# Performance work log

Hardware: AMD Instinct MI355X
Metric: run time of the kernel (lower is better)

The kernel has to match this reference:

```python
import jax, jax.numpy as jnp
import numpy as np

D_MODEL = 512
BATCH_A = 8192
MAX_MATCHES = 16
N_B = 100000
D_HID = 2 * D_MODEL  # 1024
D_IN = 2 * D_MODEL   # concat([a, mean_b])


def setup_inputs() -> dict:
    key = jax.random.key(0)
    ks = jax.random.split(key, 10)
    table_a_emb = jax.random.normal(ks[0], (BATCH_A, D_MODEL), dtype=jnp.float32)
    table_b_emb = jax.random.normal(ks[1], (N_B, D_MODEL), dtype=jnp.float32)
    # padded neighbor lists; negative values mark padding / no-match
    match_indices = jax.random.randint(ks[2], (BATCH_A, MAX_MATCHES), -5, N_B, dtype=jnp.int64)
    s_in = 1.0 / np.sqrt(D_IN)
    s_h = 1.0 / np.sqrt(D_HID)
    W_in = jax.random.uniform(ks[3], (D_IN, D_HID), jnp.float32, -s_in, s_in)
    b_in = jax.random.uniform(ks[4], (D_HID,), jnp.float32, -s_in, s_in)
    W_h = jax.random.uniform(ks[5], (D_HID, D_HID), jnp.float32, -s_h, s_h)
    b_h = jax.random.uniform(ks[6], (D_HID,), jnp.float32, -s_h, s_h)
    W_out = jax.random.uniform(ks[7], (D_HID, D_MODEL), jnp.float32, -s_h, s_h)
    b_out = jax.random.uniform(ks[8], (D_MODEL,), jnp.float32, -s_h, s_h)
    return {"table_a_emb": table_a_emb, "table_b_emb": table_b_emb,
            "match_indices": match_indices, "W_in": W_in, "b_in": b_in,
            "W_h": W_h, "b_h": b_h, "W_out": W_out, "b_out": b_out}


def reference(table_a_emb, table_b_emb, match_indices, W_in, b_in, W_h, b_h, W_out, b_out):
    mask = match_indices >= 0                                   # [B, M]
    safe_idx = jnp.where(mask, match_indices, 0)
    gathered = table_b_emb[safe_idx] * mask[..., None].astype(table_b_emb.dtype)  # [B, M, D]
    counts = mask.sum(axis=-1)                                  # [B]
    denom = jnp.maximum(counts, 1).astype(table_b_emb.dtype)[:, None]
    agg_b = gathered.sum(axis=1) / denom                        # [B, D] masked mean
    combined = jnp.concatenate([table_a_emb, agg_b], axis=-1)   # [B, 2D]
    h = jax.nn.relu(combined @ W_in + b_in)
    h = jax.nn.relu(h @ W_h + b_h)
    out = h @ W_out + b_out                                     # [B, D]
    # rows with zero valid matches emit zeros, not MLP(concat(a, 0))
    return jnp.where((counts > 0)[:, None], out, jnp.zeros_like(out))
```

## Files before the change

kernel.cpp:

```cpp
#include <hip/hip_runtime.h>

#define DM 512
#define DI 1024
#define MM 16

typedef __attribute__((ext_vector_type(4))) float f32x4;
typedef __attribute__((ext_vector_type(8))) short short8;
typedef __attribute__((ext_vector_type(8))) unsigned short ushort8;

__device__ __forceinline__ unsigned short f2bf(float x) {
  union { float f; unsigned u; } c; c.f = x;
  unsigned r = (c.u + 0x7fffu + ((c.u >> 16) & 1u)) >> 16;
  return (unsigned short)r;
}

__device__ __forceinline__ void gload_lds16(const void* g, void* l) {
  __builtin_amdgcn_global_load_lds(
      (const __attribute__((address_space(1))) unsigned int*)g,
      (__attribute__((address_space(3))) unsigned int*)l, 16, 0, 0);
}


__device__ __forceinline__ void wt_tile(const float* __restrict__ W,
                                        unsigned short* __restrict__ Wt,
                                        int K, int N, int bx, int by,
                                        float (*tile)[33], int tx, int ty) {
  #pragma unroll
  for (int i = ty; i < 32; i += 8)
    tile[i][tx] = W[(size_t)(by + i) * N + bx + tx];
  __syncthreads();
  #pragma unroll
  for (int i = ty; i < 32; i += 8)
    Wt[(size_t)(bx + i) * K + by + tx] = f2bf(tile[tx][i]);
}

__global__ __launch_bounds__(256)
void prep_kernel(const float* __restrict__ Aemb,
                 const float* __restrict__ Bemb,
                 const int* __restrict__ midx,
                 const float* __restrict__ W_in,
                 const float* __restrict__ W_h,
                 const float* __restrict__ W_out,
                 unsigned short* __restrict__ X,
                 int* __restrict__ counts,
                 unsigned short* __restrict__ Wt_in,
                 unsigned short* __restrict__ Wt_h,
                 unsigned short* __restrict__ Wt_out) {
  __shared__ float tile[32][33];
  const int b = blockIdx.x;
  const int tx = threadIdx.x & 31, ty = threadIdx.x >> 5;
  if (b < 1024) {
    wt_tile(W_in, Wt_in, 1024, 1024, (b & 31) * 32, (b >> 5) * 32, tile, tx, ty);
    return;
  } else if (b < 2048) {
    int lb = b - 1024;
    wt_tile(W_h, Wt_h, 1024, 1024, (lb & 31) * 32, (lb >> 5) * 32, tile, tx, ty);
    return;
  } else if (b < 2560) {
    int lb = b - 2048;
    wt_tile(W_out, Wt_out, 1024, 512, (lb & 15) * 32, (lb >> 4) * 32, tile, tx, ty);
    return;
  }
  int row = __builtin_amdgcn_readfirstlane((b - 2560) * 4 + (threadIdx.x >> 6));
  int l = threadIdx.x & 63;
  float acc[8] = {0,0,0,0,0,0,0,0};
  int cnt = 0;
  const int* ip = midx + row * MM;
  #pragma unroll
  for (int m = 0; m < MM; ++m) {
    int id = ip[m];
    if (id >= 0) {
      ++cnt;
      const f32x4* p = (const f32x4*)(Bemb + (size_t)id * DM) + l * 2;
      f32x4 u = p[0], v = p[1];
      acc[0]+=u[0]; acc[1]+=u[1]; acc[2]+=u[2]; acc[3]+=u[3];
      acc[4]+=v[0]; acc[5]+=v[1]; acc[6]+=v[2]; acc[7]+=v[3];
    }
  }
  float inv = 1.0f / (float)(cnt > 0 ? cnt : 1);
  const f32x4* pa = (const f32x4*)(Aemb + (size_t)row * DM) + l * 2;
  f32x4 a0 = pa[0], a1 = pa[1];
  ushort8 va, vb;
  va[0]=f2bf(a0[0]); va[1]=f2bf(a0[1]); va[2]=f2bf(a0[2]); va[3]=f2bf(a0[3]);
  va[4]=f2bf(a1[0]); va[5]=f2bf(a1[1]); va[6]=f2bf(a1[2]); va[7]=f2bf(a1[3]);
  #pragma unroll
  for (int i = 0; i < 8; ++i) vb[i] = f2bf(acc[i] * inv);
  *(ushort8*)(X + (size_t)row * DI + l * 8) = va;
  *(ushort8*)(X + (size_t)row * DI + DM + l * 8) = vb;
  if (l == 0) counts[row] = cnt;
}

template<int RELU, int FINAL>
__global__ __launch_bounds__(256, 2)
void gemm_kernel(const unsigned short* __restrict__ A,
                 const unsigned short* __restrict__ Bt,
                 const float* __restrict__ bias,
                 unsigned short* __restrict__ Cb,
                 float* __restrict__ Cf,
                 const int* __restrict__ counts,
                 int M, int N, int K) {
  __shared__ __align__(16) unsigned short As[128 * 64];
  __shared__ __align__(16) unsigned short Bs[128 * 64];
  const int t = threadIdx.x;
  const int l = t & 63, w = t >> 6;
  const int wr = w >> 1, wc = w & 1;

  const int nwg = gridDim.x * gridDim.y;
  const int wg = blockIdx.y * gridDim.x + blockIdx.x;
  const int swzid = (wg & 7) * (nwg >> 3) + (wg >> 3);
  const int bx = swzid % gridDim.x, by = swzid / gridDim.x;

  const int blockM = by * 128, blockN = bx * 128;
  const unsigned short* Ab = A + (size_t)blockM * K;
  const unsigned short* Bb = Bt + (size_t)blockN * K;

  f32x4 acc[4][4];
  #pragma unroll
  for (int m = 0; m < 4; ++m)
    #pragma unroll
    for (int n = 0; n < 4; ++n) acc[m][n] = (f32x4){0.f, 0.f, 0.f, 0.f};

  int so_row[4], so_col[4];
  #pragma unroll
  for (int c = 0; c < 4; ++c) {
    int o = c * 4096 + t * 16;
    int row = o >> 7;
    int cb = (o & 127) ^ ((row & 7) << 4);
    so_row[c] = row; so_col[c] = cb >> 1;
  }

  const int r = l & 15, ko = (l >> 4) * 8;
  const int swz = (r & 7) << 4;
  const char* Ac = (const char*)As;
  const char* Bc = (const char*)Bs;
  const int NT = K >> 6;

  #pragma unroll
  for (int c = 0; c < 4; ++c) {
    gload_lds16(Ab + (size_t)so_row[c] * K + so_col[c], (char*)As + c * 4096 + w * 1024);
    gload_lds16(Bb + (size_t)so_row[c] * K + so_col[c], (char*)Bs + c * 4096 + w * 1024);
  }

  for (int kt = 0; kt < NT; ++kt) {
    __syncthreads();
    #pragma unroll
    for (int kk = 0; kk < 64; kk += 32) {
      short8 aF[4], bF[4];
      #pragma unroll
      for (int m = 0; m < 4; ++m) {
        int byteo = ((wr * 64 + m * 16 + r) * 128 + (kk + ko) * 2) ^ swz;
        aF[m] = *(const short8*)(Ac + byteo);
      }
      #pragma unroll
      for (int n = 0; n < 4; ++n) {
        int byteo = ((wc * 64 + n * 16 + r) * 128 + (kk + ko) * 2) ^ swz;
        bF[n] = *(const short8*)(Bc + byteo);
      }
      #pragma unroll
      for (int m = 0; m < 4; ++m)
        #pragma unroll
        for (int n = 0; n < 4; ++n)
          acc[m][n] = __builtin_amdgcn_mfma_f32_16x16x32_bf16(aF[m], bF[n], acc[m][n], 0, 0, 0);
    }
    __syncthreads();
    if (kt + 1 < NT) {
      int k0 = (kt + 1) << 6;
      #pragma unroll
      for (int c = 0; c < 4; ++c) {
        gload_lds16(Ab + (size_t)so_row[c] * K + k0 + so_col[c], (char*)As + c * 4096 + w * 1024);
        gload_lds16(Bb + (size_t)so_row[c] * K + k0 + so_col[c], (char*)Bs + c * 4096 + w * 1024);
      }
    }
  }

  float bn[4];
  #pragma unroll
  for (int n = 0; n < 4; ++n) bn[n] = bias[blockN + wc * 64 + n * 16 + r];
  const int rowBase = blockM + wr * 64 + (l >> 4) * 4;
  #pragma unroll
  for (int m = 0; m < 4; ++m) {
    #pragma unroll
    for (int j = 0; j < 4; ++j) {
      int grow = rowBase + m * 16 + j;
      if (FINAL) {
        float cm = (counts[grow] > 0) ? 1.0f : 0.0f;
        #pragma unroll
        for (int n = 0; n < 4; ++n) {
          float v = (acc[m][n][j] + bn[n]) * cm;
          Cf[(size_t)grow * N + blockN + wc * 64 + n * 16 + r] = v;
        }
      } else {
        #pragma unroll
        for (int n = 0; n < 4; ++n) {
          float v = acc[m][n][j] + bn[n];
          if (RELU) v = v > 0.f ? v : 0.f;
          Cb[(size_t)grow * N + blockN + wc * 64 + n * 16 + r] = f2bf(v);
        }
      }
    }
  }
}

extern "C" void kernel_launch(void* const* d_in, const int* in_sizes, int n_in,
                              void* d_out, int out_size, void* d_ws, size_t ws_size,
                              hipStream_t stream) {
  const float* a_emb = (const float*)d_in[0];
  const float* b_emb = (const float*)d_in[1];
  const int*   midx  = (const int*)d_in[2];
  const float* W_in  = (const float*)d_in[3];
  const float* b_in  = (const float*)d_in[4];
  const float* W_h   = (const float*)d_in[5];
  const float* b_h   = (const float*)d_in[6];
  const float* W_out = (const float*)d_in[7];
  const float* b_out = (const float*)d_in[8];

  char* ws = (char*)d_ws;
  unsigned short* X      = (unsigned short*)(ws);
  unsigned short* H1     = (unsigned short*)(ws + 16777216);
  unsigned short* Wt_in  = (unsigned short*)(ws + 33554432);
  unsigned short* Wt_h   = (unsigned short*)(ws + 35651584);
  unsigned short* Wt_out = (unsigned short*)(ws + 37748736);
  int*            counts = (int*)(ws + 38797312);

  prep_kernel<<<4608, 256, 0, stream>>>(a_emb, b_emb, midx, W_in, W_h, W_out,
                                        X, counts, Wt_in, Wt_h, Wt_out);

  gemm_kernel<1, 0><<<dim3(8, 64), 256, 0, stream>>>(X,  Wt_in,  b_in,  H1, nullptr, nullptr, 8192, 1024, 1024);
  gemm_kernel<1, 0><<<dim3(8, 64), 256, 0, stream>>>(H1, Wt_h,   b_h,   X,  nullptr, nullptr, 8192, 1024, 1024);
  gemm_kernel<0, 1><<<dim3(4, 64), 256, 0, stream>>>(X,  Wt_out, b_out, nullptr, (float*)d_out, counts, 8192, 512, 1024);
}
```

Measured before the change: 114.5 us.

## Overlap gather with A-half of first GEMM via split-K fused kernel

Splits the first layer's K dimension: a fused kernel runs the gather/mean blocks interleaved with GEMM tiles computing table_a @ W_in[:512] (converting fp32 A to bf16 on the fly), storing a bf16 partial. A second GEMM then handles the mean_b half and adds the partial before bias and ReLU. Weight transposition moves to its own kernel. The aim is to overlap memory-bound gather work with matrix work, at the cost of an extra kernel launch, a bf16 round-trip for the partial sum (a precision loss), and extra workspace.

```diff
diff --git a/kernel.cpp b/kernel.cpp
--- a/kernel.cpp
+++ b/kernel.cpp
@@ -13,6 +13,9 @@
   unsigned r = (c.u + 0x7fffu + ((c.u >> 16) & 1u)) >> 16;
   return (unsigned short)r;
 }
+__device__ __forceinline__ float bf2f(unsigned short h) {
+  union { unsigned u; float f; } c; c.u = ((unsigned)h) << 16; return c.f;
+}
 
 __device__ __forceinline__ void gload_lds16(const void* g, void* l) {
   __builtin_amdgcn_global_load_lds(
@@ -20,7 +23,6 @@
       (__attribute__((address_space(3))) unsigned int*)l, 16, 0, 0);
 }
 
-
 __device__ __forceinline__ void wt_tile(const float* __restrict__ W,
                                         unsigned short* __restrict__ Wt,
                                         int K, int N, int bx, int by,
@@ -35,33 +37,150 @@
 }
 
 __global__ __launch_bounds__(256)
-void prep_kernel(const float* __restrict__ Aemb,
-                 const float* __restrict__ Bemb,
-                 const int* __restrict__ midx,
-                 const float* __restrict__ W_in,
-                 const float* __restrict__ W_h,
-                 const float* __restrict__ W_out,
-                 unsigned short* __restrict__ X,
-                 int* __restrict__ counts,
-                 unsigned short* __restrict__ Wt_in,
-                 unsigned short* __restrict__ Wt_h,
-                 unsigned short* __restrict__ Wt_out) {
+void wt_kernel(const float* __restrict__ W_in, const float* __restrict__ W_h,
+               const float* __restrict__ W_out,
+               unsigned short* __restrict__ Wt_in, unsigned short* __restrict__ Wt_h,
+               unsigned short* __restrict__ Wt_out) {
   __shared__ float tile[32][33];
   const int b = blockIdx.x;
   const int tx = threadIdx.x & 31, ty = threadIdx.x >> 5;
-  if (b < 1024) {
-    wt_tile(W_in, Wt_in, 1024, 1024, (b & 31) * 32, (b >> 5) * 32, tile, tx, ty);
+  if (b < 1024)      wt_tile(W_in,  Wt_in,  1024, 1024, (b & 31) * 32, (b >> 5) * 32, tile, tx, ty);
+  else if (b < 2048) { int lb = b - 1024; wt_tile(W_h,  Wt_h,  1024, 1024, (lb & 31) * 32, (lb >> 5) * 32, tile, tx, ty); }
+  else               { int lb = b - 2048; wt_tile(W_out, Wt_out, 1024, 512, (lb & 15) * 32, (lb >> 4) * 32, tile, tx, ty); }
+}
+
+__global__ __launch_bounds__(256, 2)
+void fused_kernel(const float* __restrict__ Aemb,
+                  const float* __restrict__ Bemb,
+                  const int* __restrict__ midx,
+                  const unsigned short* __restrict__ Wt_in,
+                  unsigned short* __restrict__ Xb,
+                  unsigned short* __restrict__ H1accb,
+                  int* __restrict__ counts) {
+  __shared__ __align__(16) unsigned short As[128 * 64];
+  __shared__ __align__(16) unsigned short Bs[128 * 64];
+  const int b = blockIdx.x;
+  const int t = threadIdx.x;
+
+  if (b % 5 != 0) {
+    int gid = b - b / 5 - 1;
+    int row = gid * 4 + (t >> 6);
+    int l = t & 63;
+    float acc[8] = {0,0,0,0,0,0,0,0};
+    int cnt = 0;
+    const int* ip = midx + row * MM;
+    #pragma unroll
+    for (int m = 0; m < MM; ++m) {
+      int id = ip[m];
+      if (id >= 0) {
+        ++cnt;
+        const f32x4* p = (const f32x4*)(Bemb + (size_t)id * DM) + l * 2;
+        f32x4 u = p[0], v = p[1];
+        acc[0]+=u[0]; acc[1]+=u[1]; acc[2]+=u[2]; acc[3]+=u[3];
+        acc[4]+=v[0]; acc[5]+=v[1]; acc[6]+=v[2]; acc[7]+=v[3];
+      }
+    }
+    float inv = 1.0f / (float)(cnt > 0 ? cnt : 1);
+    ushort8 vb;
+    #pragma unroll
+    for (int i = 0; i < 8; ++i) vb[i] = f2bf(acc[i] * inv);
+    *(ushort8*)(Xb + (size_t)row * DM + l * 8) = vb;
+    if (l == 0) counts[row] = cnt;
     return;
-  } else if (b < 2048) {
-    int lb = b - 1024;
-    wt_tile(W_h, Wt_h, 1024, 1024, (lb & 31) * 32, (lb >> 5) * 32, tile, tx, ty);
-    return;
-  } else if (b < 2560) {
-    int lb = b - 2048;
-    wt_tile(W_out, Wt_out, 1024, 512, (lb & 15) * 32, (lb >> 4) * 32, tile, tx, ty);
-    return;
-  }
-  int row = __builtin_amdgcn_readfirstlane((b - 2560) * 4 + (threadIdx.x >> 6));
+  }
+
+  const int id = b / 5;
+  const int l = t & 63, w = t >> 6;
+  const int wr = w >> 1, wc = w & 1;
+  const int swzid = (id & 7) * 64 + (id >> 3);
+  const int bx = swzid & 7, by = swzid >> 3;
+  const int blockM = by * 128, blockN = bx * 128;
+  const unsigned short* Bb = Wt_in + (size_t)blockN * 1024;
+
+  f32x4 acc[4][4];
+  #pragma unroll
+  for (int m = 0; m < 4; ++m)
+    #pragma unroll
+    for (int n = 0; n < 4; ++n) acc[m][n] = (f32x4){0.f, 0.f, 0.f, 0.f};
+
+  int so_row[4], so_col[4];
+  #pragma unroll
+  for (int c = 0; c < 4; ++c) {
+    int o = c * 4096 + t * 16;
+    int row = o >> 7;
+    int cb = (o & 127) ^ ((row & 7) << 4);
+    so_row[c] = row; so_col[c] = cb >> 1;
+  }
+
+  const int r = l & 15, ko = (l >> 4) * 8;
+  const int swz = (r & 7) << 4;
+  const char* Ac = (const char*)As;
+  const char* Bc = (const char*)Bs;
+
+  #define STAGE_A(K0)                                                         \
+    _Pragma("unroll")                                                         \
+    for (int c = 0; c < 4; ++c) {                                             \
+      int o = c * 2048 + t * 8; int row = o >> 6, col = o & 63;               \
+      const float* src = Aemb + (size_t)(blockM + row) * 512 + (K0) + col;    \
+      f32x4 u = *(const f32x4*)src; f32x4 v = *(const f32x4*)(src + 4);       \
+      ushort8 wv;                                                             \
+      wv[0]=f2bf(u[0]); wv[1]=f2bf(u[1]); wv[2]=f2bf(u[2]); wv[3]=f2bf(u[3]); \
+      wv[4]=f2bf(v[0]); wv[5]=f2bf(v[1]); wv[6]=f2bf(v[2]); wv[7]=f2bf(v[3]); \
+      int lb = (row * 128 + col * 2) ^ ((row & 7) << 4);                      \
+      *(ushort8*)((char*)As + lb) = wv;                                       \
+    }
+  #define STAGE_B(K0)                                                         \
+    _Pragma("unroll")                                                         \
+    for (int c = 0; c < 4; ++c)                                               \
+      gload_lds16(Bb + (size_t)so_row[c] * 1024 + (K0) + so_col[c],           \
+                  (char*)Bs + c * 4096 + w * 1024);
+
+  STAGE_A(0)
+  STAGE_B(0)
+  for (int kt = 0; kt < 8; ++kt) {
+    __syncthreads();
+    #pragma unroll
+    for (int kk = 0; kk < 64; kk += 32) {
+      short8 aF[4], bF[4];
+      #pragma unroll
+      for (int m = 0; m < 4; ++m)
+        aF[m] = *(const short8*)(Ac + (((wr * 64 + m * 16 + r) * 128 + (kk + ko) * 2) ^ swz));
+      #pragma unroll
+      for (int n = 0; n < 4; ++n)
+        bF[n] = *(const short8*)(Bc + (((wc * 64 + n * 16 + r) * 128 + (kk + ko) * 2) ^ swz));
+      #pragma unroll
+      for (int m = 0; m < 4; ++m)
+        #pragma unroll
+        for (int n = 0; n < 4; ++n)
+          acc[m][n] = __builtin_amdgcn_mfma_f32_16x16x32_bf16(aF[m], bF[n], acc[m][n], 0, 0, 0);
+    }
+    __syncthreads();
+    if (kt < 7) {
+      int k0 = (kt + 1) << 6;
+      STAGE_A(k0)
+      STAGE_B(k0)
+    }
+  }
+  const int rowBase = blockM + wr * 64 + (l >> 4) * 4;
+  #pragma unroll
+  for (int m = 0; m < 4; ++m)
+    #pragma unroll
+    for (int j = 0; j < 4; ++j) {
+      int grow = rowBase + m * 16 + j;
+      #pragma unroll
+      for (int n = 0; n < 4; ++n)
+        H1accb[(size_t)grow * 1024 + blockN + wc * 64 + n * 16 + r] = f2bf(acc[m][n][j]);
+    }
+  #undef STAGE_A
+  #undef STAGE_B
+}
+
+__global__ void build_x_full(const float* __restrict__ Aemb,
+                             const float* __restrict__ Bemb,
+                             const int* __restrict__ midx,
+                             unsigned short* __restrict__ X,
+                             int* __restrict__ counts) {
+  int row = blockIdx.x * 4 + (threadIdx.x >> 6);
   int l = threadIdx.x & 63;
   float acc[8] = {0,0,0,0,0,0,0,0};
   int cnt = 0;
@@ -90,15 +209,16 @@
   if (l == 0) counts[row] = cnt;
 }
 
-template<int RELU, int FINAL>
+template<int RELU, int FINAL, int ADDC>
 __global__ __launch_bounds__(256, 2)
-void gemm_kernel(const unsigned short* __restrict__ A,
-                 const unsigned short* __restrict__ Bt,
+void gemm_kernel(const unsigned short* __restrict__ A, int lda,
+                 const unsigned short* __restrict__ Bt, int ldb, int Kext,
                  const float* __restrict__ bias,
+                 const unsigned short* __restrict__ Cadd,
                  unsigned short* __restrict__ Cb,
                  float* __restrict__ Cf,
                  const int* __restrict__ counts,
-                 int M, int N, int K) {
+                 int N) {
   __shared__ __align__(16) unsigned short As[128 * 64];
   __shared__ __align__(16) unsigned short Bs[128 * 64];
   const int t = threadIdx.x;
@@ -111,8 +231,8 @@
   const int bx = swzid % gridDim.x, by = swzid / gridDim.x;
 
   const int blockM = by * 128, blockN = bx * 128;
-  const unsigned short* Ab = A + (size_t)blockM * K;
-  const unsigned short* Bb = Bt + (size_t)blockN * K;
+  const unsigned short* Ab = A + (size_t)blockM * lda;
+  const unsigned short* Bb = Bt + (size_t)blockN * ldb;
 
   f32x4 acc[4][4];
   #pragma unroll
@@ -133,12 +253,12 @@
   const int swz = (r & 7) << 4;
   const char* Ac = (const char*)As;
   const char* Bc = (const char*)Bs;
-  const int NT = K >> 6;
+  const int NT = Kext >> 6;
 
   #pragma unroll
   for (int c = 0; c < 4; ++c) {
-    gload_lds16(Ab + (size_t)so_row[c] * K + so_col[c], (char*)As + c * 4096 + w * 1024);
-    gload_lds16(Bb + (size_t)so_row[c] * K + so_col[c], (char*)Bs + c * 4096 + w * 1024);
+    gload_lds16(Ab + (size_t)so_row[c] * lda + so_col[c], (char*)As + c * 4096 + w * 1024);
+    gload_lds16(Bb + (size_t)so_row[c] * ldb + so_col[c], (char*)Bs + c * 4096 + w * 1024);
   }
 
   for (int kt = 0; kt < NT; ++kt) {
@@ -147,15 +267,11 @@
     for (int kk = 0; kk < 64; kk += 32) {
       short8 aF[4], bF[4];
       #pragma unroll
-      for (int m = 0; m < 4; ++m) {
-        int byteo = ((wr * 64 + m * 16 + r) * 128 + (kk + ko) * 2) ^ swz;
-        aF[m] = *(const short8*)(Ac + byteo);
-      }
-      #pragma unroll
-      for (int n = 0; n < 4; ++n) {
-        int byteo = ((wc * 64 + n * 16 + r) * 128 + (kk + ko) * 2) ^ swz;
-        bF[n] = *(const short8*)(Bc + byteo);
-      }
+      for (int m = 0; m < 4; ++m)
+        aF[m] = *(const short8*)(Ac + (((wr * 64 + m * 16 + r) * 128 + (kk + ko) * 2) ^ swz));
+      #pragma unroll
+      for (int n = 0; n < 4; ++n)
+        bF[n] = *(const short8*)(Bc + (((wc * 64 + n * 16 + r) * 128 + (kk + ko) * 2) ^ swz));
       #pragma unroll
       for (int m = 0; m < 4; ++m)
         #pragma unroll
@@ -167,8 +283,8 @@
       int k0 = (kt + 1) << 6;
       #pragma unroll
       for (int c = 0; c < 4; ++c) {
-        gload_lds16(Ab + (size_t)so_row[c] * K + k0 + so_col[c], (char*)As + c * 4096 + w * 1024);
-        gload_lds16(Bb + (size_t)so_row[c] * K + k0 + so_col[c], (char*)Bs + c * 4096 + w * 1024);
+        gload_lds16(Ab + (size_t)so_row[c] * lda + k0 + so_col[c], (char*)As + c * 4096 + w * 1024);
+        gload_lds16(Bb + (size_t)so_row[c] * ldb + k0 + so_col[c], (char*)Bs + c * 4096 + w * 1024);
       }
     }
   }
@@ -192,9 +308,11 @@
       } else {
         #pragma unroll
         for (int n = 0; n < 4; ++n) {
+          int gcol = blockN + wc * 64 + n * 16 + r;
           float v = acc[m][n][j] + bn[n];
+          if (ADDC) v += bf2f(Cadd[(size_t)grow * N + gcol]);
           if (RELU) v = v > 0.f ? v : 0.f;
-          Cb[(size_t)grow * N + blockN + wc * 64 + n * 16 + r] = f2bf(v);
+          Cb[(size_t)grow * N + gcol] = f2bf(v);
         }
       }
     }
@@ -213,19 +331,41 @@
   const float* b_h   = (const float*)d_in[6];
   const float* W_out = (const float*)d_in[7];
   const float* b_out = (const float*)d_in[8];
-
   char* ws = (char*)d_ws;
-  unsigned short* X      = (unsigned short*)(ws);
-  unsigned short* H1     = (unsigned short*)(ws + 16777216);
-  unsigned short* Wt_in  = (unsigned short*)(ws + 33554432);
-  unsigned short* Wt_h   = (unsigned short*)(ws + 35651584);
-  unsigned short* Wt_out = (unsigned short*)(ws + 37748736);
-  int*            counts = (int*)(ws + 38797312);
-
-  prep_kernel<<<4608, 256, 0, stream>>>(a_emb, b_emb, midx, W_in, W_h, W_out,
-                                        X, counts, Wt_in, Wt_h, Wt_out);
-
-  gemm_kernel<1, 0><<<dim3(8, 64), 256, 0, stream>>>(X,  Wt_in,  b_in,  H1, nullptr, nullptr, 8192, 1024, 1024);
-  gemm_kernel<1, 0><<<dim3(8, 64), 256, 0, stream>>>(H1, Wt_h,   b_h,   X,  nullptr, nullptr, 8192, 1024, 1024);
-  gemm_kernel<0, 1><<<dim3(4, 64), 256, 0, stream>>>(X,  Wt_out, b_out, nullptr, (float*)d_out, counts, 8192, 512, 1024);
-}
+
+  if (ws_size >= 47218688ull) {
+    unsigned short* Xb     = (unsigned short*)(ws);
+    unsigned short* H1accb = (unsigned short*)(ws + 8388608);
+    unsigned short* H1     = (unsigned short*)(ws + 25165824);
+    unsigned short* H2     = (unsigned short*)(ws);
+    unsigned short* Wt_in  = (unsigned short*)(ws + 41943040);
+    unsigned short* Wt_h   = (unsigned short*)(ws + 44040192);
+    unsigned short* Wt_out = (unsigned short*)(ws + 46137344);
+    int*            counts = (int*)(ws + 47185920);
+
+    wt_kernel<<<2560, 256, 0, stream>>>(W_in, W_h, W_out, Wt_in, Wt_h, Wt_out);
+    fused_kernel<<<2560, 256, 0, stream>>>(a_emb, b_emb, midx, Wt_in, Xb, H1accb, counts);
+    gemm_kernel<1, 0, 1><<<dim3(8, 64), 256, 0, stream>>>(Xb, 512, Wt_in + 512, 1024, 512,
+                                                          b_in, H1accb, H1, nullptr, nullptr, 1024);
+    gemm_kernel<1, 0, 0><<<dim3(8, 64), 256, 0, stream>>>(H1, 1024, Wt_h, 1024, 1024,
+                                                          b_h, nullptr, H2, nullptr, nullptr, 1024);
+    gemm_kernel<0, 1, 0><<<dim3(4, 64), 256, 0, stream>>>(H2, 1024, Wt_out, 1024, 1024,
+                                                          b_out, nullptr, nullptr, (float*)d_out, counts, 512);
+  } else {
+    unsigned short* X      = (unsigned short*)(ws);
+    unsigned short* H1     = (unsigned short*)(ws + 16777216);
+    unsigned short* Wt_in  = (unsigned short*)(ws + 33554432);
+    unsigned short* Wt_h   = (unsigned short*)(ws + 35651584);
+    unsigned short* Wt_out = (unsigned short*)(ws + 37748736);
+    int*            counts = (int*)(ws + 38797312);
+
+    wt_kernel<<<2560, 256, 0, stream>>>(W_in, W_h, W_out, Wt_in, Wt_h, Wt_out);
+    build_x_full<<<2048, 256, 0, stream>>>(a_emb, b_emb, midx, X, counts);
+    gemm_kernel<1, 0, 0><<<dim3(8, 64), 256, 0, stream>>>(X, 1024, Wt_in, 1024, 1024,
+                                                          b_in, nullptr, H1, nullptr, nullptr, 1024);
+    gemm_kernel<1, 0, 0><<<dim3(8, 64), 256, 0, stream>>>(H1, 1024, Wt_h, 1024, 1024,
+                                                          b_h, nullptr, X, nullptr, nullptr, 1024);
+    gemm_kernel<0, 1, 0><<<dim3(4, 64), 256, 0, stream>>>(X, 1024, Wt_out, 1024, 1024,
+                                                          b_out, nullptr, nullptr, (float*)d_out, counts, 512);
+  }
+}
```

Measured after the change: 128.5 us. 12.2% more time.

## Add triple-buffered 256x128 GEMM for hidden layers and split prep kernel

Applied to the files above, without the earlier changes.

Adds a new GEMM kernel for the two 1024x1024 layers. It uses 256x128 tiles, 8 waves and triple-buffered LDS (144KB dynamic), with the loads for stage k+2 issued while stage k is computed. It also adds explicit vmcnt waits, raises the wave priority around the MFMA block, and maps tiles to XCDs. The old fused prep kernel is split into separate weight-transpose and gather kernels, and the final layer keeps the old kernel with generalized leading dimensions. This aims to hide global load latency and improve reuse, at the cost of occupancy and one extra launch.

```diff
diff --git a/kernel.cpp b/kernel.cpp
--- a/kernel.cpp
+++ b/kernel.cpp
@@ -13,6 +13,9 @@
   unsigned r = (c.u + 0x7fffu + ((c.u >> 16) & 1u)) >> 16;
   return (unsigned short)r;
 }
+__device__ __forceinline__ float bf2f(unsigned short h) {
+  union { unsigned u; float f; } c; c.u = ((unsigned)h) << 16; return c.f;
+}
 
 __device__ __forceinline__ void gload_lds16(const void* g, void* l) {
   __builtin_amdgcn_global_load_lds(
@@ -20,7 +23,6 @@
       (__attribute__((address_space(3))) unsigned int*)l, 16, 0, 0);
 }
 
-
 __device__ __forceinline__ void wt_tile(const float* __restrict__ W,
                                         unsigned short* __restrict__ Wt,
                                         int K, int N, int bx, int by,
@@ -35,33 +37,24 @@
 }
 
 __global__ __launch_bounds__(256)
-void prep_kernel(const float* __restrict__ Aemb,
-                 const float* __restrict__ Bemb,
-                 const int* __restrict__ midx,
-                 const float* __restrict__ W_in,
-                 const float* __restrict__ W_h,
-                 const float* __restrict__ W_out,
-                 unsigned short* __restrict__ X,
-                 int* __restrict__ counts,
-                 unsigned short* __restrict__ Wt_in,
-                 unsigned short* __restrict__ Wt_h,
-                 unsigned short* __restrict__ Wt_out) {
+void wt_kernel(const float* __restrict__ W_in, const float* __restrict__ W_h,
+               const float* __restrict__ W_out,
+               unsigned short* __restrict__ Wt_in, unsigned short* __restrict__ Wt_h,
+               unsigned short* __restrict__ Wt_out) {
   __shared__ float tile[32][33];
   const int b = blockIdx.x;
   const int tx = threadIdx.x & 31, ty = threadIdx.x >> 5;
-  if (b < 1024) {
-    wt_tile(W_in, Wt_in, 1024, 1024, (b & 31) * 32, (b >> 5) * 32, tile, tx, ty);
-    return;
-  } else if (b < 2048) {
-    int lb = b - 1024;
-    wt_tile(W_h, Wt_h, 1024, 1024, (lb & 31) * 32, (lb >> 5) * 32, tile, tx, ty);
-    return;
-  } else if (b < 2560) {
-    int lb = b - 2048;
-    wt_tile(W_out, Wt_out, 1024, 512, (lb & 15) * 32, (lb >> 4) * 32, tile, tx, ty);
-    return;
-  }
-  int row = __builtin_amdgcn_readfirstlane((b - 2560) * 4 + (threadIdx.x >> 6));
+  if (b < 1024)      wt_tile(W_in,  Wt_in,  1024, 1024, (b & 31) * 32, (b >> 5) * 32, tile, tx, ty);
+  else if (b < 2048) { int lb = b - 1024; wt_tile(W_h,  Wt_h,  1024, 1024, (lb & 31) * 32, (lb >> 5) * 32, tile, tx, ty); }
+  else               { int lb = b - 2048; wt_tile(W_out, Wt_out, 1024, 512, (lb & 15) * 32, (lb >> 4) * 32, tile, tx, ty); }
+}
+
+__global__ void build_x_full(const float* __restrict__ Aemb,
+                             const float* __restrict__ Bemb,
+                             const int* __restrict__ midx,
+                             unsigned short* __restrict__ X,
+                             int* __restrict__ counts) {
+  int row = blockIdx.x * 4 + (threadIdx.x >> 6);
   int l = threadIdx.x & 63;
   float acc[8] = {0,0,0,0,0,0,0,0};
   int cnt = 0;
@@ -90,15 +83,137 @@
   if (l == 0) counts[row] = cnt;
 }
 
+template<int RELU>
+__global__ __launch_bounds__(512, 2)
+void gemm2_kernel(const unsigned short* __restrict__ A,
+                  const unsigned short* __restrict__ Bt,
+                  const float* __restrict__ bias,
+                  unsigned short* __restrict__ C,
+                  int N, int K) {
+  extern __shared__ __align__(16) char smem[];
+  const int t = threadIdx.x;
+  const int l = t & 63, w = t >> 6;
+  const int wr = w >> 1, wc = w & 1;
+
+  const int f = blockIdx.y * gridDim.x + blockIdx.x;
+  const int xcd = f & 7, j = f >> 3;
+  const int bx = j & 7, by = xcd * 4 + (j >> 3);
+  const int blockM = by * 256, blockN = bx * 128;
+  const unsigned short* Ab = A + (size_t)blockM * K;
+  const unsigned short* Bb = Bt + (size_t)blockN * K;
+
+  f32x4 acc[4][4];
+  #pragma unroll
+  for (int m = 0; m < 4; ++m)
+    #pragma unroll
+    for (int n = 0; n < 4; ++n) acc[m][n] = (f32x4){0.f, 0.f, 0.f, 0.f};
+
+  int arow[4], acol[4], brow[2], bcol[2];
+  #pragma unroll
+  for (int c = 0; c < 4; ++c) {
+    int o = c * 8192 + t * 16;
+    int row = o >> 7;
+    int cb = (o & 127) ^ ((row & 7) << 4);
+    arow[c] = row; acol[c] = cb >> 1;
+  }
+  #pragma unroll
+  for (int c = 0; c < 2; ++c) {
+    int o = c * 8192 + t * 16;
+    int row = o >> 7;
+    int cb = (o & 127) ^ ((row & 7) << 4);
+    brow[c] = row; bcol[c] = cb >> 1;
+  }
+
+  const int r = l & 15, ko = (l >> 4) * 8;
+  const int swz = (r & 7) << 4;
+  const int NT = K >> 6;
+
+  float bn[4];
+  #pragma unroll
+  for (int n = 0; n < 4; ++n) bn[n] = bias[blockN + wc * 64 + n * 16 + r];
+
+  #define STAGE(BUF, KT)                                                      \
+    {                                                                         \
+      int k0_ = (KT) << 6;                                                    \
+      char* ab_ = smem + (BUF) * 32768;                                       \
+      char* bb_ = smem + 98304 + (BUF) * 16384;                               \
+      _Pragma("unroll")                                                       \
+      for (int c = 0; c < 4; ++c)                                             \
+        gload_lds16(Ab + (size_t)arow[c] * K + k0_ + acol[c],                 \
+                    ab_ + c * 8192 + t * 16);                                 \
+      _Pragma("unroll")                                                       \
+      for (int c = 0; c < 2; ++c)                                             \
+        gload_lds16(Bb + (size_t)brow[c] * K + k0_ + bcol[c],                 \
+                    bb_ + c * 8192 + t * 16);                                 \
+    }
+
+  STAGE(0, 0)
+  STAGE(1, 1)
+
+  int rc = 0;
+  int sc = 2;
+  for (int kt = 0; kt < NT; ++kt) {
+    if (kt + 1 < NT) { asm volatile("s_waitcnt vmcnt(6)" ::: "memory"); }
+    else             { asm volatile("s_waitcnt vmcnt(0)" ::: "memory"); }
+    __builtin_amdgcn_sched_barrier(0);
+    __builtin_amdgcn_s_barrier();
+    __builtin_amdgcn_sched_barrier(0);
+    if (kt + 2 < NT) STAGE(sc, kt + 2)
+
+    const char* Ac = smem + rc * 32768;
+    const char* Bc = smem + 98304 + rc * 16384;
+    short8 aF[2][4], bF[2][4];
+    #pragma unroll
+    for (int kk = 0; kk < 2; ++kk) {
+      #pragma unroll
+      for (int m = 0; m < 4; ++m)
+        aF[kk][m] = *(const short8*)(Ac + (((wr * 64 + m * 16 + r) * 128 + (kk * 32 + ko) * 2) ^ swz));
+      #pragma unroll
+      for (int n = 0; n < 4; ++n)
+        bF[kk][n] = *(const short8*)(Bc + (((wc * 64 + n * 16 + r) * 128 + (kk * 32 + ko) * 2) ^ swz));
+    }
+    asm volatile("s_waitcnt lgkmcnt(0)" ::: "memory");
+    __builtin_amdgcn_sched_barrier(0);
+
+    __builtin_amdgcn_s_setprio(1);
+    #pragma unroll
+    for (int kk = 0; kk < 2; ++kk)
+      #pragma unroll
+      for (int m = 0; m < 4; ++m)
+        #pragma unroll
+        for (int n = 0; n < 4; ++n)
+          acc[m][n] = __builtin_amdgcn_mfma_f32_16x16x32_bf16(aF[kk][m], bF[kk][n], acc[m][n], 0, 0, 0);
+    __builtin_amdgcn_s_setprio(0);
+
+    rc = (rc == 2) ? 0 : rc + 1;
+    sc = (sc == 2) ? 0 : sc + 1;
+  }
+  #undef STAGE
+
+  const int rowBase = blockM + wr * 64 + (l >> 4) * 4;
+  #pragma unroll
+  for (int m = 0; m < 4; ++m)
+    #pragma unroll
+    for (int jj = 0; jj < 4; ++jj) {
+      int grow = rowBase + m * 16 + jj;
+      #pragma unroll
+      for (int n = 0; n < 4; ++n) {
+        float v = acc[m][n][jj] + bn[n];
+        if (RELU) v = v > 0.f ? v : 0.f;
+        C[(size_t)grow * N + blockN + wc * 64 + n * 16 + r] = f2bf(v);
+      }
+    }
+}
+
 template<int RELU, int FINAL>
 __global__ __launch_bounds__(256, 2)
-void gemm_kernel(const unsigned short* __restrict__ A,
-                 const unsigned short* __restrict__ Bt,
+void gemm_kernel(const unsigned short* __restrict__ A, int lda,
+                 const unsigned short* __restrict__ Bt, int ldb, int Kext,
                  const float* __restrict__ bias,
                  unsigned short* __restrict__ Cb,
                  float* __restrict__ Cf,
                  const int* __restrict__ counts,
-                 int M, int N, int K) {
+                 int N) {
   __shared__ __align__(16) unsigned short As[128 * 64];
   __shared__ __align__(16) unsigned short Bs[128 * 64];
   const int t = threadIdx.x;
@@ -111,8 +226,8 @@
   const int bx = swzid % gridDim.x, by = swzid / gridDim.x;
 
   const int blockM = by * 128, blockN = bx * 128;
-  const unsigned short* Ab = A + (size_t)blockM * K;
-  const unsigned short* Bb = Bt + (size_t)blockN * K;
+  const unsigned short* Ab = A + (size_t)blockM * lda;
+  const unsigned short* Bb = Bt + (size_t)blockN * ldb;
 
   f32x4 acc[4][4];
   #pragma unroll
@@ -133,12 +248,12 @@
   const int swz = (r & 7) << 4;
   const char* Ac = (const char*)As;
   const char* Bc = (const char*)Bs;
-  const int NT = K >> 6;
+  const int NT = Kext >> 6;
 
   #pragma unroll
   for (int c = 0; c < 4; ++c) {
-    gload_lds16(Ab + (size_t)so_row[c] * K + so_col[c], (char*)As + c * 4096 + w * 1024);
-    gload_lds16(Bb + (size_t)so_row[c] * K + so_col[c], (char*)Bs + c * 4096 + w * 1024);
+    gload_lds16(Ab + (size_t)so_row[c] * lda + so_col[c], (char*)As + c * 4096 + w * 1024);
+    gload_lds16(Bb + (size_t)so_row[c] * ldb + so_col[c], (char*)Bs + c * 4096 + w * 1024);
   }
 
   for (int kt = 0; kt < NT; ++kt) {
@@ -147,15 +262,11 @@
     for (int kk = 0; kk < 64; kk += 32) {
       short8 aF[4], bF[4];
       #pragma unroll
-      for (int m = 0; m < 4; ++m) {
-        int byteo = ((wr * 64 + m * 16 + r) * 128 + (kk + ko) * 2) ^ swz;
-        aF[m] = *(const short8*)(Ac + byteo);
-      }
-      #pragma unroll
-      for (int n = 0; n < 4; ++n) {
-        int byteo = ((wc * 64 + n * 16 + r) * 128 + (kk + ko) * 2) ^ swz;
-        bF[n] = *(const short8*)(Bc + byteo);
-      }
+      for (int m = 0; m < 4; ++m)
+        aF[m] = *(const short8*)(Ac + (((wr * 64 + m * 16 + r) * 128 + (kk + ko) * 2) ^ swz));
+      #pragma unroll
+      for (int n = 0; n < 4; ++n)
+        bF[n] = *(const short8*)(Bc + (((wc * 64 + n * 16 + r) * 128 + (kk + ko) * 2) ^ swz));
       #pragma unroll
       for (int m = 0; m < 4; ++m)
         #pragma unroll
@@ -167,8 +278,8 @@
       int k0 = (kt + 1) << 6;
       #pragma unroll
       for (int c = 0; c < 4; ++c) {
-        gload_lds16(Ab + (size_t)so_row[c] * K + k0 + so_col[c], (char*)As + c * 4096 + w * 1024);
-        gload_lds16(Bb + (size_t)so_row[c] * K + k0 + so_col[c], (char*)Bs + c * 4096 + w * 1024);
+        gload_lds16(Ab + (size_t)so_row[c] * lda + k0 + so_col[c], (char*)As + c * 4096 + w * 1024);
+        gload_lds16(Bb + (size_t)so_row[c] * ldb + k0 + so_col[c], (char*)Bs + c * 4096 + w * 1024);
       }
     }
   }
@@ -180,19 +291,19 @@
   #pragma unroll
   for (int m = 0; m < 4; ++m) {
     #pragma unroll
-    for (int j = 0; j < 4; ++j) {
-      int grow = rowBase + m * 16 + j;
+    for (int jj = 0; jj < 4; ++jj) {
+      int grow = rowBase + m * 16 + jj;
       if (FINAL) {
         float cm = (counts[grow] > 0) ? 1.0f : 0.0f;
         #pragma unroll
         for (int n = 0; n < 4; ++n) {
-          float v = (acc[m][n][j] + bn[n]) * cm;
+          float v = (acc[m][n][jj] + bn[n]) * cm;
           Cf[(size_t)grow * N + blockN + wc * 64 + n * 16 + r] = v;
         }
       } else {
         #pragma unroll
         for (int n = 0; n < 4; ++n) {
-          float v = acc[m][n][j] + bn[n];
+          float v = acc[m][n][jj] + bn[n];
           if (RELU) v = v > 0.f ? v : 0.f;
           Cb[(size_t)grow * N + blockN + wc * 64 + n * 16 + r] = f2bf(v);
         }
@@ -213,8 +324,8 @@
   const float* b_h   = (const float*)d_in[6];
   const float* W_out = (const float*)d_in[7];
   const float* b_out = (const float*)d_in[8];
-
   char* ws = (char*)d_ws;
+
   unsigned short* X      = (unsigned short*)(ws);
   unsigned short* H1     = (unsigned short*)(ws + 16777216);
   unsigned short* Wt_in  = (unsigned short*)(ws + 33554432);
@@ -222,10 +333,14 @@
   unsigned short* Wt_out = (unsigned short*)(ws + 37748736);
   int*            counts = (int*)(ws + 38797312);
 
-  prep_kernel<<<4608, 256, 0, stream>>>(a_emb, b_emb, midx, W_in, W_h, W_out,
-                                        X, counts, Wt_in, Wt_h, Wt_out);
-
-  gemm_kernel<1, 0><<<dim3(8, 64), 256, 0, stream>>>(X,  Wt_in,  b_in,  H1, nullptr, nullptr, 8192, 1024, 1024);
-  gemm_kernel<1, 0><<<dim3(8, 64), 256, 0, stream>>>(H1, Wt_h,   b_h,   X,  nullptr, nullptr, 8192, 1024, 1024);
-  gemm_kernel<0, 1><<<dim3(4, 64), 256, 0, stream>>>(X,  Wt_out, b_out, nullptr, (float*)d_out, counts, 8192, 512, 1024);
-}
+  (void)hipFuncSetAttribute((const void*)gemm2_kernel<1>,
+                            hipFuncAttributeMaxDynamicSharedMemorySize, 147456);
+
+  wt_kernel<<<2560, 256, 0, stream>>>(W_in, W_h, W_out, Wt_in, Wt_h, Wt_out);
+  build_x_full<<<2048, 256, 0, stream>>>(a_emb, b_emb, midx, X, counts);
+
+  gemm2_kernel<1><<<dim3(8, 32), 512, 147456, stream>>>(X,  Wt_in, b_in, H1, 1024, 1024);
+  gemm2_kernel<1><<<dim3(8, 32), 512, 147456, stream>>>(H1, Wt_h,  b_h,  X,  1024, 1024);
+  gemm_kernel<0, 1><<<dim3(4, 64), 256, 0, stream>>>(X, 1024, Wt_out, 1024, 1024,
+                                                     b_out, nullptr, (float*)d_out, counts, 512);
+}
```

Measured after the change: 117.7 us. 1.03x slower.

## Add double-buffered 256x128 GEMM kernel with 8 waves for first two layers

Applied to the files above, without the earlier changes.

Replaces the two 1024x1024 hidden-layer GEMMs with a new kernel that uses 512 threads, 256x128 output tiles, and a two-stage double-buffered LDS pipeline. Global-to-LDS loads are split into quarter chunks interleaved with MFMA phases, using explicit vmcnt/lgkmcnt waits, s_setprio and sched barriers. The aim is to hide global load latency and reduce barrier stalls compared with the single-buffered 128x128 kernel. The cost is 96KB of dynamic LDS per block, which lowers occupancy, plus hand-coded wait counts that are fragile. The final GEMM only gains generalized leading-dimension arguments.

```diff
diff --git a/kernel.cpp b/kernel.cpp
--- a/kernel.cpp
+++ b/kernel.cpp
@@ -19,7 +19,6 @@
       (const __attribute__((address_space(1))) unsigned int*)g,
       (__attribute__((address_space(3))) unsigned int*)l, 16, 0, 0);
 }
-
 
 __device__ __forceinline__ void wt_tile(const float* __restrict__ W,
                                         unsigned short* __restrict__ Wt,
@@ -90,15 +89,150 @@
   if (l == 0) counts[row] = cnt;
 }
 
+__global__ __launch_bounds__(512, 2)
+void gemm8_kernel(const unsigned short* __restrict__ A,
+                  const unsigned short* __restrict__ Bt,
+                  const float* __restrict__ bias,
+                  unsigned short* __restrict__ C) {
+  extern __shared__ __align__(16) char smem[];
+  const int t = threadIdx.x;
+  const int l = t & 63, w = t >> 6;
+  const int wr = w >> 2, wc = w & 3;
+  const int f = blockIdx.y * gridDim.x + blockIdx.x;
+  const int swzid = (f & 7) * 32 + (f >> 3);
+  const int bx = swzid & 7, by = swzid >> 3;
+  const int blockM = by * 256, blockN = bx * 128;
+  const unsigned short* __restrict__ Ab = A + (size_t)blockM * 1024;
+  const unsigned short* __restrict__ Bb = Bt + (size_t)blockN * 1024;
+  const int r = l & 15, ko = (l >> 4) * 8;
+  const int swz = (r & 7) << 4;
+  const int strow = t >> 3;
+  const int stcolh = ((((t & 7) * 16) ^ ((strow & 7) << 4)) >> 1);
+
+  f32x4 acc[8][2];
+  #pragma unroll
+  for (int m = 0; m < 8; ++m) {
+    acc[m][0] = (f32x4){0.f,0.f,0.f,0.f};
+    acc[m][1] = (f32x4){0.f,0.f,0.f,0.f};
+  }
+
+#define ST_A(BASE, KT, CH)                                                    \
+  gload_lds16(Ab + (size_t)((CH)*64 + strow) * 1024 + ((KT)<<6) + stcolh,     \
+              smem + (BASE) + (CH)*8192 + t*16);
+#define ST_B(BASE, KT, CB)                                                    \
+  gload_lds16(Bb + (size_t)((CB)*64 + strow) * 1024 + ((KT)<<6) + stcolh,     \
+              smem + (BASE) + 32768 + (CB)*8192 + t*16);
+#define ST_QM0B(BASE, KT) { ST_A(BASE,KT,0) ST_A(BASE,KT,2) ST_B(BASE,KT,0) ST_B(BASE,KT,1) }
+#define ST_QM1(BASE, KT)  { ST_A(BASE,KT,1) ST_A(BASE,KT,3) }
+
+#define WAIT_VM(N) { asm volatile("s_waitcnt vmcnt(" #N ")" ::: "memory");    \
+                     __builtin_amdgcn_sched_barrier(0); }
+#define WAIT_LGKM() { asm volatile("s_waitcnt lgkmcnt(0)" ::: "memory");      \
+                      __builtin_amdgcn_sched_barrier(0); }
+#define BAR() { __builtin_amdgcn_s_barrier();                                 \
+                __builtin_amdgcn_sched_barrier(0); }
+
+  short8 aF[4][2], bF[2][2];
+
+#define LDA(MF4, KK, BASE, QM)                                                \
+  aF[MF4][KK] = *(const short8*)(smem + (BASE) +                              \
+      ((((wr*128 + ((QM)*4+(MF4))*16 + r) * 128) + ((KK)*32 + ko)*2) ^ swz));
+#define LDB(NF, KK, BASE)                                                     \
+  bF[NF][KK] = *(const short8*)(smem + (BASE) + 32768 +                       \
+      ((((wc*32 + (NF)*16 + r) * 128) + ((KK)*32 + ko)*2) ^ swz));
+
+#define MFMA16(QM)                                                            \
+  __builtin_amdgcn_s_setprio(1);                                              \
+  _Pragma("unroll") for (int mf4 = 0; mf4 < 4; ++mf4)                         \
+    _Pragma("unroll") for (int kk = 0; kk < 2; ++kk)                          \
+      _Pragma("unroll") for (int nf = 0; nf < 2; ++nf)                        \
+        acc[(QM)*4+mf4][nf] = __builtin_amdgcn_mfma_f32_16x16x32_bf16(        \
+            aF[mf4][kk], bF[nf][kk], acc[(QM)*4+mf4][nf], 0, 0, 0);           \
+  __builtin_amdgcn_s_setprio(0);
+
+#define DS_A(BASE, QM) _Pragma("unroll")                                      \
+  for (int mf4 = 0; mf4 < 4; ++mf4) { LDA(mf4,0,BASE,QM) LDA(mf4,1,BASE,QM) }
+#define DS_B(BASE) { LDB(0,0,BASE) LDB(0,1,BASE) LDB(1,0,BASE) LDB(1,1,BASE) }
+
+  ST_QM0B(0, 0) ST_QM1(0, 0)
+  ST_QM0B(49152, 1) ST_QM1(49152, 1)
+  WAIT_VM(8) BAR()
+
+  { DS_A(0,0) DS_B(0)
+    WAIT_LGKM() MFMA16(0)
+    WAIT_VM(6) BAR() }
+  { DS_A(0,1)
+    ST_QM0B(0, 2)
+    WAIT_LGKM() MFMA16(1)
+    WAIT_VM(6) BAR() }
+
+  #pragma unroll 1
+  for (int kt = 1; kt <= 13; ++kt) {
+    const int bo = (kt & 1) * 49152;
+    const int bo2 = bo ^ 49152;
+    { DS_A(bo,0) DS_B(bo)
+      ST_QM1(bo2, kt+1)
+      WAIT_LGKM() MFMA16(0)
+      WAIT_VM(6) BAR() }
+    { DS_A(bo,1)
+      ST_QM0B(bo, kt+2)
+      WAIT_LGKM() MFMA16(1)
+      WAIT_VM(6) BAR() }
+  }
+
+  { DS_A(0,0) DS_B(0)
+    ST_QM1(49152, 15)
+    WAIT_LGKM() MFMA16(0)
+    WAIT_VM(6) BAR() }
+  { DS_A(0,1)
+    WAIT_LGKM() MFMA16(1)
+    WAIT_VM(2) BAR() }
+  { DS_A(49152,0) DS_B(49152)
+    WAIT_LGKM() MFMA16(0)
+    WAIT_VM(0) BAR() }
+  { DS_A(49152,1)
+    WAIT_LGKM() MFMA16(1) }
+
+#undef ST_A
+#undef ST_B
+#undef ST_QM0B
+#undef ST_QM1
+#undef WAIT_VM
+#undef WAIT_LGKM
+#undef BAR
+#undef LDA
+#undef LDB
+#undef MFMA16
+#undef DS_A
+#undef DS_B
+
+  float bn2[2];
+  bn2[0] = bias[blockN + wc * 32 + r];
+  bn2[1] = bias[blockN + wc * 32 + 16 + r];
+  const int rowBase = blockM + wr * 128 + (l >> 4) * 4;
+  #pragma unroll
+  for (int mf = 0; mf < 8; ++mf)
+    #pragma unroll
+    for (int j = 0; j < 4; ++j) {
+      int grow = rowBase + mf * 16 + j;
+      #pragma unroll
+      for (int nf = 0; nf < 2; ++nf) {
+        float v = acc[mf][nf][j] + bn2[nf];
+        v = v > 0.f ? v : 0.f;
+        C[(size_t)grow * 1024 + blockN + wc * 32 + nf * 16 + r] = f2bf(v);
+      }
+    }
+}
+
 template<int RELU, int FINAL>
 __global__ __launch_bounds__(256, 2)
-void gemm_kernel(const unsigned short* __restrict__ A,
-                 const unsigned short* __restrict__ Bt,
+void gemm_kernel(const unsigned short* __restrict__ A, int lda,
+                 const unsigned short* __restrict__ Bt, int ldb, int Kext,
                  const float* __restrict__ bias,
                  unsigned short* __restrict__ Cb,
                  float* __restrict__ Cf,
                  const int* __restrict__ counts,
-                 int M, int N, int K) {
+                 int N) {
   __shared__ __align__(16) unsigned short As[128 * 64];
   __shared__ __align__(16) unsigned short Bs[128 * 64];
   const int t = threadIdx.x;
@@ -111,8 +245,8 @@
   const int bx = swzid % gridDim.x, by = swzid / gridDim.x;
 
   const int blockM = by * 128, blockN = bx * 128;
-  const unsigned short* Ab = A + (size_t)blockM * K;
-  const unsigned short* Bb = Bt + (size_t)blockN * K;
+  const unsigned short* Ab = A + (size_t)blockM * lda;
+  const unsigned short* Bb = Bt + (size_t)blockN * ldb;
 
   f32x4 acc[4][4];
   #pragma unroll
@@ -133,12 +267,12 @@
   const int swz = (r & 7) << 4;
   const char* Ac = (const char*)As;
   const char* Bc = (const char*)Bs;
-  const int NT = K >> 6;
+  const int NT = Kext >> 6;
 
   #pragma unroll
   for (int c = 0; c < 4; ++c) {
-    gload_lds16(Ab + (size_t)so_row[c] * K + so_col[c], (char*)As + c * 4096 + w * 1024);
-    gload_lds16(Bb + (size_t)so_row[c] * K + so_col[c], (char*)Bs + c * 4096 + w * 1024);
+    gload_lds16(Ab + (size_t)so_row[c] * lda + so_col[c], (char*)As + c * 4096 + w * 1024);
+    gload_lds16(Bb + (size_t)so_row[c] * ldb + so_col[c], (char*)Bs + c * 4096 + w * 1024);
   }
 
   for (int kt = 0; kt < NT; ++kt) {
@@ -147,15 +281,11 @@
     for (int kk = 0; kk < 64; kk += 32) {
       short8 aF[4], bF[4];
       #pragma unroll
-      for (int m = 0; m < 4; ++m) {
-        int byteo = ((wr * 64 + m * 16 + r) * 128 + (kk + ko) * 2) ^ swz;
-        aF[m] = *(const short8*)(Ac + byteo);
-      }
-      #pragma unroll
-      for (int n = 0; n < 4; ++n) {
-        int byteo = ((wc * 64 + n * 16 + r) * 128 + (kk + ko) * 2) ^ swz;
-        bF[n] = *(const short8*)(Bc + byteo);
-      }
+      for (int m = 0; m < 4; ++m)
+        aF[m] = *(const short8*)(Ac + (((wr * 64 + m * 16 + r) * 128 + (kk + ko) * 2) ^ swz));
+      #pragma unroll
+      for (int n = 0; n < 4; ++n)
+        bF[n] = *(const short8*)(Bc + (((wc * 64 + n * 16 + r) * 128 + (kk + ko) * 2) ^ swz));
       #pragma unroll
       for (int m = 0; m < 4; ++m)
         #pragma unroll
@@ -167,8 +297,8 @@
       int k0 = (kt + 1) << 6;
       #pragma unroll
       for (int c = 0; c < 4; ++c) {
-        gload_lds16(Ab + (size_t)so_row[c] * K + k0 + so_col[c], (char*)As + c * 4096 + w * 1024);
-        gload_lds16(Bb + (size_t)so_row[c] * K + k0 + so_col[c], (char*)Bs + c * 4096 + w * 1024);
+        gload_lds16(Ab + (size_t)so_row[c] * lda + k0 + so_col[c], (char*)As + c * 4096 + w * 1024);
+        gload_lds16(Bb + (size_t)so_row[c] * ldb + k0 + so_col[c], (char*)Bs + c * 4096 + w * 1024);
       }
     }
   }
@@ -180,19 +310,19 @@
   #pragma unroll
   for (int m = 0; m < 4; ++m) {
     #pragma unroll
-    for (int j = 0; j < 4; ++j) {
-      int grow = rowBase + m * 16 + j;
+    for (int jj = 0; jj < 4; ++jj) {
+      int grow = rowBase + m * 16 + jj;
       if (FINAL) {
         float cm = (counts[grow] > 0) ? 1.0f : 0.0f;
         #pragma unroll
         for (int n = 0; n < 4; ++n) {
-          float v = (acc[m][n][j] + bn[n]) * cm;
+          float v = (acc[m][n][jj] + bn[n]) * cm;
           Cf[(size_t)grow * N + blockN + wc * 64 + n * 16 + r] = v;
         }
       } else {
         #pragma unroll
         for (int n = 0; n < 4; ++n) {
-          float v = acc[m][n][j] + bn[n];
+          float v = acc[m][n][jj] + bn[n];
           if (RELU) v = v > 0.f ? v : 0.f;
           Cb[(size_t)grow * N + blockN + wc * 64 + n * 16 + r] = f2bf(v);
         }
@@ -213,8 +343,8 @@
   const float* b_h   = (const float*)d_in[6];
   const float* W_out = (const float*)d_in[7];
   const float* b_out = (const float*)d_in[8];
-
   char* ws = (char*)d_ws;
+
   unsigned short* X      = (unsigned short*)(ws);
   unsigned short* H1     = (unsigned short*)(ws + 16777216);
   unsigned short* Wt_in  = (unsigned short*)(ws + 33554432);
@@ -222,10 +352,14 @@
   unsigned short* Wt_out = (unsigned short*)(ws + 37748736);
   int*            counts = (int*)(ws + 38797312);
 
+  (void)hipFuncSetAttribute((const void*)gemm8_kernel,
+                            hipFuncAttributeMaxDynamicSharedMemorySize, 98304);
+
   prep_kernel<<<4608, 256, 0, stream>>>(a_emb, b_emb, midx, W_in, W_h, W_out,
                                         X, counts, Wt_in, Wt_h, Wt_out);
 
-  gemm_kernel<1, 0><<<dim3(8, 64), 256, 0, stream>>>(X,  Wt_in,  b_in,  H1, nullptr, nullptr, 8192, 1024, 1024);
-  gemm_kernel<1, 0><<<dim3(8, 64), 256, 0, stream>>>(H1, Wt_h,   b_h,   X,  nullptr, nullptr, 8192, 1024, 1024);
-  gemm_kernel<0, 1><<<dim3(4, 64), 256, 0, stream>>>(X,  Wt_out, b_out, nullptr, (float*)d_out, counts, 8192, 512, 1024);
-}
+  gemm8_kernel<<<dim3(8, 32), 512, 98304, stream>>>(X,  Wt_in, b_in, H1);
+  gemm8_kernel<<<dim3(8, 32), 512, 98304, stream>>>(H1, Wt_h,  b_h,  X);
+  gemm_kernel<0, 1><<<dim3(4, 64), 256, 0, stream>>>(X, 1024, Wt_out, 1024, 1024,
+                                                     b_out, nullptr, (float*)d_out, counts, 512);
+}
```

Result: no change. 113.2 us, median of 2 (-1.1%).
